# Optimization experiments

Measured on AMD Instinct MI355X. Metric: run time of the kernel, lower is better.

The kernel has to match this reference:

```python
import jax, jax.numpy as jnp
import numpy as np

OUT_F, IN_F = 4096, 11008
NUMEL = OUT_F * IN_F            # divisible by 256
NUM_SUPER = NUMEL // 256        # super-blocks of 8 sub-blocks x 32 values


def setup_inputs() -> dict:
    key = jax.random.key(0)
    k = jax.random.split(key, 7)
    x = jax.random.normal(k[0], (64, IN_F), dtype=jnp.float32)
    packed = jax.random.randint(k[1], (NUMEL // 2,), 0, 256, dtype=jnp.int32)
    d = jax.random.uniform(k[2], (NUM_SUPER,), dtype=jnp.float32) * 0.02
    dmin = jax.random.uniform(k[3], (NUM_SUPER,), dtype=jnp.float32) * 0.02
    scales = jax.random.randint(k[4], (NUM_SUPER * 8,), 0, 64, dtype=jnp.int32)
    mins = jax.random.randint(k[5], (NUM_SUPER * 8,), 0, 64, dtype=jnp.int32)
    bias = jax.random.normal(k[6], (OUT_F,), dtype=jnp.float32) * 0.02
    return {"x": x, "packed": packed, "d": d, "dmin": dmin,
            "scales": scales, "mins": mins, "bias": bias}


def _dequant_q4k(packed, d, dmin, scales, mins):
    # unpack two 4-bit quants per byte, interleaved low/high (stack dim=1 + flatten)
    low = packed & 15
    high = (packed >> 4) & 15
    q = jnp.stack([low, high], axis=1).reshape(NUM_SUPER, 8, 32).astype(jnp.float32)
    sc = (scales.astype(jnp.float32) / 63.0).reshape(NUM_SUPER, 8, 1)
    mn = (mins.astype(jnp.float32) / 63.0).reshape(NUM_SUPER, 8, 1)
    normalized = q / 15.0 * sc + mn
    w = normalized * d.reshape(NUM_SUPER, 1, 1) + dmin.reshape(NUM_SUPER, 1, 1)
    return w.reshape(OUT_F, IN_F)


def reference(x, packed, d, dmin, scales, mins, bias):
    w = _dequant_q4k(packed, d, dmin, scales, mins)   # [OUT_F, IN_F] fp32
    return x @ w.T + bias                              # F.linear
```

## Files before the change

kernel.cpp:

```cpp
#include <hip/hip_runtime.h>
#include <stdint.h>

#define OUT_F   4096
#define IN_F    11008
#define BATCH   64
#define NSUP    43
#define SB_ROW  344
#define IPR     5504
#define NKS     16
#define XP_BYTES   (4 * 344 * 64 * 16)
#define PART_ELEMS ((size_t)NKS * BATCH * OUT_F)
#define WS_FULL    (XP_BYTES + PART_ELEMS * 4)

typedef __attribute__((ext_vector_type(8))) short  short8;
typedef __attribute__((ext_vector_type(4))) float  floatx4;
typedef __attribute__((ext_vector_type(4))) int    intx4;

__device__ __forceinline__ unsigned pack_bf16(float f0, float f1) {
    return __builtin_amdgcn_perm(__float_as_uint(f1), __float_as_uint(f0), 0x07060302u);
}

__global__ __launch_bounds__(256) void xprep_kernel(const float* __restrict__ x,
                                                    intx4* __restrict__ xp) {
    const int ksb = blockIdx.x;
    const int mt  = threadIdx.x >> 6;
    const int l   = threadIdx.x & 63;
    const int lo  = l & 15, hi = l >> 4;
    const float* src = x + (mt * 16 + lo) * IN_F + ksb * 32 + hi * 8;
    floatx4 a0 = *(const floatx4*)src;
    floatx4 a1 = *(const floatx4*)(src + 4);
    intx4 r;
    r.x = pack_bf16(a0.x, a0.y);
    r.y = pack_bf16(a0.z, a0.w);
    r.z = pack_bf16(a1.x, a1.y);
    r.w = pack_bf16(a1.z, a1.w);
    xp[(mt * 344 + ksb) * 64 + l] = r;
}

__global__ __launch_bounds__(256) void init_out_kernel(const float* __restrict__ bias,
                                                       float* __restrict__ out) {
    int i = blockIdx.x * 256 + threadIdx.x;
    out[i] = bias[i & (OUT_F - 1)];
}

__global__ __launch_bounds__(256) void reduce_kernel(const float* __restrict__ part,
                                                     const float* __restrict__ bias,
                                                     float* __restrict__ out) {
    const int i = blockIdx.x * 256 + threadIdx.x;
    float s = bias[i & (OUT_F - 1)];
    #pragma unroll
    for (int k = 0; k < NKS; ++k) s += part[(size_t)k * (BATCH * OUT_F) + i];
    out[i] = s;
}

template<bool USE_XP, bool USE_PART>
__global__ __launch_bounds__(256, 4) void qlin_main(
    const float* __restrict__ x,
    const intx4* __restrict__ xp,
    const int*   __restrict__ packed,
    const float* __restrict__ dd,
    const float* __restrict__ dmn_g,
    const int*   __restrict__ scales,
    const int*   __restrict__ mins,
    float*       __restrict__ part,
    float*       __restrict__ out)
{
    const int nb = blockIdx.x & 63;
    const int ks = blockIdx.x >> 6;
    const int w  = threadIdx.x >> 6;
    const int l  = threadIdx.x & 63;
    const int lo = l & 15, hi = l >> 4;

    const int o = nb * 64 + w * 16 + lo;
    const int sup0 = ks < 11 ? 3 * ks : 33 + 2 * (ks - 11);
    const int nsup = ks < 11 ? 3 : 2;

    floatx4 acc[4];
    #pragma unroll
    for (int mt = 0; mt < 4; ++mt) acc[mt] = (floatx4)0.0f;

    #pragma unroll 1
    for (int s = 0; s < nsup; ++s) {
        const int sup = sup0 + s;

        const int sci = o * SB_ROW + sup * 8;
        intx4 sc0 = *(const intx4*)(scales + sci);
        intx4 sc1 = *(const intx4*)(scales + sci + 4);
        intx4 mn0 = *(const intx4*)(mins + sci);
        intx4 mn1 = *(const intx4*)(mins + sci + 4);
        const float dv   = dd[o * NSUP + sup];
        const float dmnv = dmn_g[o * NSUP + sup];
        const float d945 = dv * (1.0f / 945.0f);
        const float d63  = dv * (1.0f / 63.0f);

        const int* bp = packed + o * IPR + sup * 128 + hi * 4;
        const intx4* xpp = xp + (sup * 8) * 64 + l;

        #pragma unroll
        for (int step = 0; step < 8; ++step) {
            intx4 braw = *(const intx4*)(bp + step * 16);

            intx4 xf[4];
            if (USE_XP) {
                #pragma unroll
                for (int mt = 0; mt < 4; ++mt)
                    xf[mt] = xpp[(mt * 344 + step) * 64];
            } else {
                #pragma unroll
                for (int mt = 0; mt < 4; ++mt) {
                    const float* src = x + (mt * 16 + lo) * IN_F + sup * 256 + step * 32 + hi * 8;
                    floatx4 a0 = *(const floatx4*)src;
                    floatx4 a1 = *(const floatx4*)(src + 4);
                    xf[mt].x = pack_bf16(a0.x, a0.y);
                    xf[mt].y = pack_bf16(a0.z, a0.w);
                    xf[mt].z = pack_bf16(a1.x, a1.y);
                    xf[mt].w = pack_bf16(a1.z, a1.w);
                }
            }

            const int sc = (step < 4) ? sc0[step & 3] : sc1[step & 3];
            const int mn = (step < 4) ? mn0[step & 3] : mn1[step & 3];
            const float A = d945 * (float)sc;
            const float B = fmaf(d63, (float)mn, dmnv);

            union { intx4 i; short8 s; } uw;
            {
                const int v0 = braw.x, v1 = braw.y, v2 = braw.z, v3 = braw.w;
                uw.i.x = pack_bf16(fmaf((float)(v0 & 15), A, B), fmaf((float)(v0 >> 4), A, B));
                uw.i.y = pack_bf16(fmaf((float)(v1 & 15), A, B), fmaf((float)(v1 >> 4), A, B));
                uw.i.z = pack_bf16(fmaf((float)(v2 & 15), A, B), fmaf((float)(v2 >> 4), A, B));
                uw.i.w = pack_bf16(fmaf((float)(v3 & 15), A, B), fmaf((float)(v3 >> 4), A, B));
            }

            union { intx4 i; short8 s; } ua0, ua1, ua2, ua3;
            ua0.i = xf[0]; ua1.i = xf[1]; ua2.i = xf[2]; ua3.i = xf[3];
            acc[0] = __builtin_amdgcn_mfma_f32_16x16x32_bf16(ua0.s, uw.s, acc[0], 0, 0, 0);
            acc[1] = __builtin_amdgcn_mfma_f32_16x16x32_bf16(ua1.s, uw.s, acc[1], 0, 0, 0);
            acc[2] = __builtin_amdgcn_mfma_f32_16x16x32_bf16(ua2.s, uw.s, acc[2], 0, 0, 0);
            acc[3] = __builtin_amdgcn_mfma_f32_16x16x32_bf16(ua3.s, uw.s, acc[3], 0, 0, 0);
        }
    }

    if (USE_PART) {
        float* pbase = part + (size_t)ks * (BATCH * OUT_F) + o;
        #pragma unroll
        for (int mt = 0; mt < 4; ++mt) {
            #pragma unroll
            for (int r = 0; r < 4; ++r)
                pbase[(mt * 16 + hi * 4 + r) * OUT_F] = acc[mt][r];
        }
    } else {
        #pragma unroll
        for (int mt = 0; mt < 4; ++mt) {
            #pragma unroll
            for (int r = 0; r < 4; ++r)
                atomicAdd(out + (mt * 16 + hi * 4 + r) * OUT_F + o, acc[mt][r]);
        }
    }
}

extern "C" void kernel_launch(void* const* d_in, const int* in_sizes, int n_in,
                              void* d_out, int out_size, void* d_ws, size_t ws_size,
                              hipStream_t stream) {
    (void)in_sizes; (void)n_in; (void)out_size;
    const float* x      = (const float*)d_in[0];
    const int*   packed = (const int*)d_in[1];
    const float* d      = (const float*)d_in[2];
    const float* dmin   = (const float*)d_in[3];
    const int*   scales = (const int*)d_in[4];
    const int*   mins   = (const int*)d_in[5];
    const float* bias   = (const float*)d_in[6];
    float* out = (float*)d_out;

    const bool has_xp   = ws_size >= (size_t)XP_BYTES;
    const bool has_part = ws_size >= (size_t)WS_FULL;
    intx4* xp   = (intx4*)d_ws;
    float* part = (float*)((char*)d_ws + XP_BYTES);

    if (has_xp)
        xprep_kernel<<<344, 256, 0, stream>>>(x, xp);

    if (has_part) {
        qlin_main<true, true><<<64 * NKS, 256, 0, stream>>>(
            x, xp, packed, d, dmin, scales, mins, part, out);
        reduce_kernel<<<(BATCH * OUT_F) / 256, 256, 0, stream>>>(part, bias, out);
    } else {
        init_out_kernel<<<(BATCH * OUT_F) / 256, 256, 0, stream>>>(bias, out);
        if (has_xp)
            qlin_main<true, false><<<64 * NKS, 256, 0, stream>>>(
                x, xp, packed, d, dmin, scales, mins, part, out);
        else
            qlin_main<false, false><<<64 * NKS, 256, 0, stream>>>(
                x, xp, packed, d, dmin, scales, mins, part, out);
    }
}
```

Measured before the change: 183.4 us.

## Software-pipeline packed weight loads with nontemporal prefetch and swap block order

Restructures the main loop into half-superblock stages that prefetch the next 4 packed-weight vectors, scales, mins and d/dmin into registers while dequantizing and running MFMAs on the current ones. Packed loads use nontemporal hints to avoid polluting cache with single-use weight data. Block index mapping is swapped so consecutive blocks share an output tile across K-splits rather than a K-split across output tiles, changing L2 locality of x prep data. The fallback non-workspace x path is removed, so xprep always runs and the workspace must be present. The extra prefetch registers raise register pressure against the 4-waves launch bound.

Result: no change. 181.5 us (-1.0%).

```diff
diff --git a/kernel.cpp b/kernel.cpp
--- a/kernel.cpp
+++ b/kernel.cpp
@@ -53,9 +53,8 @@
     out[i] = s;
 }
 
-template<bool USE_XP, bool USE_PART>
+template<bool USE_PART>
 __global__ __launch_bounds__(256, 4) void qlin_main(
-    const float* __restrict__ x,
     const intx4* __restrict__ xp,
     const int*   __restrict__ packed,
     const float* __restrict__ dd,
@@ -65,13 +64,13 @@
     float*       __restrict__ part,
     float*       __restrict__ out)
 {
-    const int nb = blockIdx.x & 63;
-    const int ks = blockIdx.x >> 6;
+    const int ks = blockIdx.x & 15;
+    const int nb = blockIdx.x >> 4;
     const int w  = threadIdx.x >> 6;
     const int l  = threadIdx.x & 63;
     const int lo = l & 15, hi = l >> 4;
 
-    const int o = nb * 64 + w * 16 + lo;
+    const int o    = nb * 64 + w * 16 + lo;
     const int sup0 = ks < 11 ? 3 * ks : 33 + 2 * (ks - 11);
     const int nsup = ks < 11 ? 3 : 2;
 
@@ -79,66 +78,71 @@
     #pragma unroll
     for (int mt = 0; mt < 4; ++mt) acc[mt] = (floatx4)0.0f;
 
+    const int* bp  = packed + o * IPR + sup0 * 128 + hi * 4;
+    const int* scp = scales + o * SB_ROW + sup0 * 8;
+    const int* mnp = mins   + o * SB_ROW + sup0 * 8;
+    int didx = o * NSUP + sup0;
+    const intx4* xpc = xp + (sup0 * 8) * 64 + l;
+
+    intx4 bc[4], bn[4], scc, mnc, scn, mnn;
+    #pragma unroll
+    for (int i = 0; i < 4; ++i)
+        bc[i] = __builtin_nontemporal_load((const intx4*)(bp + i * 16));
+    scc = *(const intx4*)scp;
+    mnc = *(const intx4*)mnp;
+    float dvc = dd[didx], dmc = dmn_g[didx];
+
+    auto do_half = [&](const intx4* bb, intx4 scv, intx4 mnv,
+                       float A945, float A63, float ADMN, const intx4* xq) {
+        #pragma unroll
+        for (int st = 0; st < 4; ++st) {
+            const int v0 = bb[st].x, v1 = bb[st].y, v2 = bb[st].z, v3 = bb[st].w;
+            const float A = A945 * (float)scv[st];
+            const float B = fmaf(A63, (float)mnv[st], ADMN);
+            union { intx4 i; short8 s; } uw;
+            uw.i.x = pack_bf16(fmaf((float)(v0 & 15), A, B), fmaf((float)(v0 >> 4), A, B));
+            uw.i.y = pack_bf16(fmaf((float)(v1 & 15), A, B), fmaf((float)(v1 >> 4), A, B));
+            uw.i.z = pack_bf16(fmaf((float)(v2 & 15), A, B), fmaf((float)(v2 >> 4), A, B));
+            uw.i.w = pack_bf16(fmaf((float)(v3 & 15), A, B), fmaf((float)(v3 >> 4), A, B));
+            union { intx4 i; short8 s; } u0, u1, u2, u3;
+            u0.i = xq[(0 * 344 + st) * 64];
+            u1.i = xq[(1 * 344 + st) * 64];
+            u2.i = xq[(2 * 344 + st) * 64];
+            u3.i = xq[(3 * 344 + st) * 64];
+            acc[0] = __builtin_amdgcn_mfma_f32_16x16x32_bf16(u0.s, uw.s, acc[0], 0, 0, 0);
+            acc[1] = __builtin_amdgcn_mfma_f32_16x16x32_bf16(u1.s, uw.s, acc[1], 0, 0, 0);
+            acc[2] = __builtin_amdgcn_mfma_f32_16x16x32_bf16(u2.s, uw.s, acc[2], 0, 0, 0);
+            acc[3] = __builtin_amdgcn_mfma_f32_16x16x32_bf16(u3.s, uw.s, acc[3], 0, 0, 0);
+        }
+    };
+
     #pragma unroll 1
-    for (int s = 0; s < nsup; ++s) {
-        const int sup = sup0 + s;
+    for (int s = 0;; ++s) {
+        const bool last = (s == nsup - 1);
+        #pragma unroll
+        for (int i = 0; i < 4; ++i)
+            bn[i] = __builtin_nontemporal_load((const intx4*)(bp + 64 + i * 16));
+        scn = *(const intx4*)(scp + 4);
+        mnn = *(const intx4*)(mnp + 4);
 
-        const int sci = o * SB_ROW + sup * 8;
-        intx4 sc0 = *(const intx4*)(scales + sci);
-        intx4 sc1 = *(const intx4*)(scales + sci + 4);
-        intx4 mn0 = *(const intx4*)(mins + sci);
-        intx4 mn1 = *(const intx4*)(mins + sci + 4);
-        const float dv   = dd[o * NSUP + sup];
-        const float dmnv = dmn_g[o * NSUP + sup];
-        const float d945 = dv * (1.0f / 945.0f);
-        const float d63  = dv * (1.0f / 63.0f);
+        const float A945 = dvc * (1.0f / 945.0f);
+        const float A63  = dvc * (1.0f / 63.0f);
+        do_half(bc, scc, mnc, A945, A63, dmc, xpc);
 
-        const int* bp = packed + o * IPR + sup * 128 + hi * 4;
-        const intx4* xpp = xp + (sup * 8) * 64 + l;
-
-        #pragma unroll
-        for (int step = 0; step < 8; ++step) {
-            intx4 braw = *(const intx4*)(bp + step * 16);
-
-            intx4 xf[4];
-            if (USE_XP) {
-                #pragma unroll
-                for (int mt = 0; mt < 4; ++mt)
-                    xf[mt] = xpp[(mt * 344 + step) * 64];
-            } else {
-                #pragma unroll
-                for (int mt = 0; mt < 4; ++mt) {
-                    const float* src = x + (mt * 16 + lo) * IN_F + sup * 256 + step * 32 + hi * 8;
-                    floatx4 a0 = *(const floatx4*)src;
-                    floatx4 a1 = *(const floatx4*)(src + 4);
-                    xf[mt].x = pack_bf16(a0.x, a0.y);
-                    xf[mt].y = pack_bf16(a0.z, a0.w);
-                    xf[mt].z = pack_bf16(a1.x, a1.y);
-                    xf[mt].w = pack_bf16(a1.z, a1.w);
-                }
-            }
-
-            const int sc = (step < 4) ? sc0[step & 3] : sc1[step & 3];
-            const int mn = (step < 4) ? mn0[step & 3] : mn1[step & 3];
-            const float A = d945 * (float)sc;
-            const float B = fmaf(d63, (float)mn, dmnv);
-
-            union { intx4 i; short8 s; } uw;
-            {
-                const int v0 = braw.x, v1 = braw.y, v2 = braw.z, v3 = braw.w;
-                uw.i.x = pack_bf16(fmaf((float)(v0 & 15), A, B), fmaf((float)(v0 >> 4), A, B));
-                uw.i.y = pack_bf16(fmaf((float)(v1 & 15), A, B), fmaf((float)(v1 >> 4), A, B));
-                uw.i.z = pack_bf16(fmaf((float)(v2 & 15), A, B), fmaf((float)(v2 >> 4), A, B));
-                uw.i.w = pack_bf16(fmaf((float)(v3 & 15), A, B), fmaf((float)(v3 >> 4), A, B));
-            }
-
-            union { intx4 i; short8 s; } ua0, ua1, ua2, ua3;
-            ua0.i = xf[0]; ua1.i = xf[1]; ua2.i = xf[2]; ua3.i = xf[3];
-            acc[0] = __builtin_amdgcn_mfma_f32_16x16x32_bf16(ua0.s, uw.s, acc[0], 0, 0, 0);
-            acc[1] = __builtin_amdgcn_mfma_f32_16x16x32_bf16(ua1.s, uw.s, acc[1], 0, 0, 0);
-            acc[2] = __builtin_amdgcn_mfma_f32_16x16x32_bf16(ua2.s, uw.s, acc[2], 0, 0, 0);
-            acc[3] = __builtin_amdgcn_mfma_f32_16x16x32_bf16(ua3.s, uw.s, acc[3], 0, 0, 0);
+        float dvn = 0.0f, dmnn = 0.0f;
+        if (!last) {
+            #pragma unroll
+            for (int i = 0; i < 4; ++i)
+                bc[i] = __builtin_nontemporal_load((const intx4*)(bp + 128 + i * 16));
+            scc = *(const intx4*)(scp + 8);
+            mnc = *(const intx4*)(mnp + 8);
+            dvn = dd[didx + 1];
+            dmnn = dmn_g[didx + 1];
         }
+        do_half(bn, scn, mnn, A945, A63, dmc, xpc + 256);
+        if (last) break;
+        dvc = dvn; dmc = dmnn; ++didx;
+        bp += 128; scp += 8; mnp += 8; xpc += 512;
     }
 
     if (USE_PART) {
@@ -172,25 +176,19 @@
     const float* bias   = (const float*)d_in[6];
     float* out = (float*)d_out;
 
-    const bool has_xp   = ws_size >= (size_t)XP_BYTES;
     const bool has_part = ws_size >= (size_t)WS_FULL;
     intx4* xp   = (intx4*)d_ws;
     float* part = (float*)((char*)d_ws + XP_BYTES);
 
-    if (has_xp)
-        xprep_kernel<<<344, 256, 0, stream>>>(x, xp);
+    xprep_kernel<<<344, 256, 0, stream>>>(x, xp);
 
     if (has_part) {
-        qlin_main<true, true><<<64 * NKS, 256, 0, stream>>>(
-            x, xp, packed, d, dmin, scales, mins, part, out);
+        qlin_main<true><<<64 * NKS, 256, 0, stream>>>(
+            xp, packed, d, dmin, scales, mins, part, out);
         reduce_kernel<<<(BATCH * OUT_F) / 256, 256, 0, stream>>>(part, bias, out);
     } else {
         init_out_kernel<<<(BATCH * OUT_F) / 256, 256, 0, stream>>>(bias, out);
-        if (has_xp)
-            qlin_main<true, false><<<64 * NKS, 256, 0, stream>>>(
-                x, xp, packed, d, dmin, scales, mins, part, out);
-        else
-            qlin_main<false, false><<<64 * NKS, 256, 0, stream>>>(
-                x, xp, packed, d, dmin, scales, mins, part, out);
+        qlin_main<false><<<64 * NKS, 256, 0, stream>>>(
+            xp, packed, d, dmin, scales, mins, part, out);
     }
 }
```
